# Kernel tuning notes

Measured on AMD Instinct MI355X. Metric: run time of the kernel, lower is better.

The kernel has to match this reference:

```python
import jax, jax.numpy as jnp
import numpy as np

DIM = 512
TEMB_DIM = 512
NUM_HEADS = 16
WS = 16  # window_size
N = WS * WS
B = 256


def _relative_position_index(ws: int) -> np.ndarray:
    """Swin-style relative position index, shape [ws*ws, ws*ws], values in [0, (2ws-1)^2)."""
    coords = np.stack(np.meshgrid(np.arange(ws), np.arange(ws), indexing='ij'))  # [2, ws, ws]
    flat = coords.reshape(2, -1)                                                  # [2, N]
    rel = flat[:, :, None] - flat[:, None, :]                                     # [2, N, N]
    rel = rel.transpose(1, 2, 0).copy()                                           # [N, N, 2]
    rel[:, :, 0] += ws - 1
    rel[:, :, 1] += ws - 1
    rel[:, :, 0] *= 2 * ws - 1
    return rel.sum(-1).astype(np.int32)


def setup_inputs() -> dict:
    key = jax.random.key(0)
    ks = jax.random.split(key, 8)
    lin = lambda k, fan_in, shape: jax.random.normal(k, shape, jnp.float32) * (1.0 / np.sqrt(fan_in))
    return {
        'x': jax.random.normal(ks[0], (B, N, DIM), jnp.float32),
        'temb': jax.random.normal(ks[1], (B, TEMB_DIM), jnp.float32),
        'qkv_w': lin(ks[2], DIM, (DIM, 3 * DIM)),
        'qkv_b': jnp.zeros((3 * DIM,), jnp.float32),
        'temb_w': lin(ks[3], TEMB_DIM, (TEMB_DIM, 3 * DIM)),
        'temb_b': jnp.zeros((3 * DIM,), jnp.float32),
        'rpb_table': jax.random.normal(ks[4], ((2 * WS - 1) ** 2, NUM_HEADS), jnp.float32) * 0.02,
        'proj_w': lin(ks[5], DIM, (DIM, DIM)),
        'proj_b': jnp.zeros((DIM,), jnp.float32),
        'rp_index': jnp.asarray(_relative_position_index(WS)),
    }


def reference(x, temb, qkv_w, qkv_b, temb_w, temb_b, rpb_table, proj_w, proj_b, rp_index):
    Bq, Nq, C = x.shape
    H = NUM_HEADS
    hd = C // H
    # qkv with time-embedding modulation: [B, N, 3C]
    qkv = x @ qkv_w + qkv_b + (temb @ temb_w + temb_b)[:, None, :]
    qkv = qkv.reshape(Bq, Nq, 3, H, hd).transpose(2, 0, 3, 1, 4)  # [3, B, H, N, hd]
    q, k, v = qkv[0], qkv[1], qkv[2]
    # relative position bias: [H, N, N]
    bias = rpb_table[rp_index.reshape(-1)].reshape(Nq, Nq, H).transpose(2, 0, 1)
    scale = 1.0 / jnp.sqrt(jnp.asarray(hd, x.dtype))  # SDPA default scale
    scores = jnp.einsum('bhqd,bhkd->bhqk', q, k) * scale + bias[None]
    attn = jax.nn.softmax(scores, axis=-1)
    out = jnp.einsum('bhqk,bhkd->bhqd', attn, v)       # [B, H, N, hd]
    out = out.transpose(0, 2, 1, 3).reshape(Bq, Nq, C)
    return out @ proj_w + proj_b
```

## Files before the change

kernel.cpp:

```cpp
#include <hip/hip_runtime.h>
#include <hip/hip_bf16.h>

#define B_ 256
#define N_ 256
#define H_ 16
#define SCALE2_ 0.25504526484f
#define LOG2E_ 1.4426950408889634f

typedef __attribute__((ext_vector_type(8))) short short8;
typedef __attribute__((ext_vector_type(4))) float f32x4v;
typedef unsigned int u32;

#define GLOAD16(gptr, lptr)                                                        \
  __builtin_amdgcn_global_load_lds((const __attribute__((address_space(1))) u32*)(gptr), \
                                   (__attribute__((address_space(3))) u32*)(lptr), 16, 0, 0)

static __device__ __forceinline__ unsigned cvt_pk_bf16(float lo, float hi) {
  unsigned r;
  asm("v_cvt_pk_bf16_f32 %0, %1, %2" : "=v"(r) : "v"(lo), "v"(hi));
  return r;
}

__global__ void cvt_x_kernel(const float* __restrict__ in, unsigned* __restrict__ out, int n8) {
  int i = blockIdx.x * 256 + threadIdx.x;
  int stride = gridDim.x * 256;
  for (; i < n8; i += stride) {
    const float4* p = reinterpret_cast<const float4*>(in + (size_t)i * 8);
    float4 a = p[0], b = p[1];
    uint4 vv = make_uint4(cvt_pk_bf16(a.x, a.y), cvt_pk_bf16(a.z, a.w),
                          cvt_pk_bf16(b.x, b.y), cvt_pk_bf16(b.z, b.w));
    *reinterpret_cast<uint4*>(out + (size_t)i * 4) = vv;
  }
}

__global__ void cvt_wT_kernel(const float* __restrict__ in, unsigned short* __restrict__ out, int ncols) {
  __shared__ float tile[32][65];
  const int nb = ncols >> 6;
  const int k0 = (blockIdx.x / nb) << 5;
  const int n0 = (blockIdx.x % nb) << 6;
  const int t = threadIdx.x;
  {
    int kk = t >> 3, c0 = (t & 7) << 3;
    const float* src = in + (size_t)(k0 + kk) * ncols + n0 + c0;
    float4 v0 = *reinterpret_cast<const float4*>(src);
    float4 v1 = *reinterpret_cast<const float4*>(src + 4);
    tile[kk][c0 + 0] = v0.x; tile[kk][c0 + 1] = v0.y; tile[kk][c0 + 2] = v0.z; tile[kk][c0 + 3] = v0.w;
    tile[kk][c0 + 4] = v1.x; tile[kk][c0 + 5] = v1.y; tile[kk][c0 + 6] = v1.z; tile[kk][c0 + 7] = v1.w;
  }
  __syncthreads();
  {
    int nn = t >> 2, c0 = (t & 3) << 3;
    uint4 vv = make_uint4(cvt_pk_bf16(tile[c0 + 0][nn], tile[c0 + 1][nn]),
                          cvt_pk_bf16(tile[c0 + 2][nn], tile[c0 + 3][nn]),
                          cvt_pk_bf16(tile[c0 + 4][nn], tile[c0 + 5][nn]),
                          cvt_pk_bf16(tile[c0 + 6][nn], tile[c0 + 7][nn]));
    *reinterpret_cast<uint4*>(out + (size_t)(n0 + nn) * 512 + k0 + c0) = vv;
  }
}

__global__ __launch_bounds__(512)
void temb_mod_kernel(const float* __restrict__ temb,
                     const float* __restrict__ temb_w,
                     const float* __restrict__ temb_b,
                     const float* __restrict__ qkv_b,
                     float* __restrict__ tm) {
  __shared__ float ts[512];
  const int b = blockIdx.x, t = threadIdx.x;
  ts[t] = temb[(size_t)b * 512 + t];
  __syncthreads();
  float a0 = temb_b[t] + qkv_b[t];
  float a1 = temb_b[t + 512] + qkv_b[t + 512];
  float a2 = temb_b[t + 1024] + qkv_b[t + 1024];
#pragma unroll 4
  for (int k = 0; k < 512; ++k) {
    const float tv = ts[k];
    const float* wr = temb_w + (size_t)k * 1536 + t;
    a0 += tv * wr[0];
    a1 += tv * wr[512];
    a2 += tv * wr[1024];
  }
  float* o = tm + (size_t)b * 1536 + t;
  o[0] = a0; o[512] = a1; o[1024] = a2;
}

__global__ __launch_bounds__(512, 4)
void fused_attn_kernel(const unsigned short* __restrict__ xb16,
                       const unsigned short* __restrict__ wT,
                       const float* __restrict__ rpb,
                       const float* __restrict__ tm,
                       unsigned short* __restrict__ attn_out) {
  __shared__ __align__(16) char smem[53008];
  short* xs  = (short*)smem;
  short* ksp = (short*)(smem + 16384);
  short* vTs = (short*)(smem + 32768);
  float* biasT = (float*)(smem + 49152);

  const int u = blockIdx.x;
  const int bh = ((u & 7) << 9) | (u >> 3);
  const int b = bh >> 4, h = bh & 15;
  const int tid = threadIdx.x;
  const int w = tid >> 6, l = tid & 63;
  const int l16 = l & 15, g = l >> 4;
  const int gsw8 = (g ^ ((l16 >> 1) & 3)) << 3;
  const int lrow = l >> 2;
  const int lcol = (((l & 3) ^ ((l >> 3) & 3)) << 3);

  const unsigned short* xsrc0 = xb16 + (size_t)(b * 256 + w * 16 + lrow) * 512 + lcol;
  const unsigned short* xsrc1 = xsrc0 + (size_t)128 * 512;
  const int row96 = w * 16 + lrow;
  const unsigned short* wsrc = wT + (size_t)((row96 >> 5) * 512 + h * 32 + (row96 & 31)) * 512 + lcol;

  f32x4v acc[2][6];
#pragma unroll
  for (int mt = 0; mt < 2; ++mt)
#pragma unroll
    for (int nt = 0; nt < 6; ++nt) acc[mt][nt] = (f32x4v)(0.0f);

  auto stage = [&](int t, int bufi) {
    const int k0 = t << 5;
    GLOAD16(xsrc0 + k0, xs + bufi * 8192 + w * 512);
    GLOAD16(xsrc1 + k0, xs + bufi * 8192 + (8 + w) * 512);
    if (w < 6) GLOAD16(wsrc + k0, xs + 16384 + bufi * 3072 + w * 512);
  };
  stage(0, 0);
  __syncthreads();
#pragma unroll
  for (int t = 0; t < 16; ++t) {
    const int cur = t & 1;
    if (t < 15) stage(t + 1, cur ^ 1);
    short* xb = xs + cur * 8192;
    short* wb = xs + 16384 + cur * 3072;
    short8 af[2], bfr[6];
#pragma unroll
    for (int mt = 0; mt < 2; ++mt)
      af[mt] = *reinterpret_cast<short8*>(&xb[(w * 32 + mt * 16 + l16) * 32 + gsw8]);
#pragma unroll
    for (int nt = 0; nt < 6; ++nt)
      bfr[nt] = *reinterpret_cast<short8*>(&wb[(nt * 16 + l16) * 32 + gsw8]);
#pragma unroll
    for (int mt = 0; mt < 2; ++mt)
#pragma unroll
      for (int nt = 0; nt < 6; ++nt)
        acc[mt][nt] = __builtin_amdgcn_mfma_f32_16x16x32_bf16(af[mt], bfr[nt], acc[mt][nt], 0, 0, 0);
    __syncthreads();
  }

  const float* tmb = tm + (size_t)b * 1536 + h * 32;
#pragma unroll
  for (int nt = 0; nt < 6; ++nt) {
    const int prt = nt >> 1;
    const int d = ((nt & 1) << 4) + l16;
    const float tmv = tmb[(prt << 9) + d];
#pragma unroll
    for (int mt = 0; mt < 2; ++mt) {
      const int r0 = w * 32 + mt * 16 + g * 4;
      float v0 = acc[mt][nt][0] + tmv, v1 = acc[mt][nt][1] + tmv;
      float v2 = acc[mt][nt][2] + tmv, v3 = acc[mt][nt][3] + tmv;
      if (prt == 0) { v0 *= SCALE2_; v1 *= SCALE2_; v2 *= SCALE2_; v3 *= SCALE2_; }
      const u32 p01 = cvt_pk_bf16(v0, v1);
      const u32 p23 = cvt_pk_bf16(v2, v3);
      if (prt != 2) {
        short* dst = (prt == 0) ? xs : ksp;
        const int unit01 = ((d >> 3) ^ ((r0 >> 1) & 3)) << 3;
        const int base = r0 * 32 + unit01 + (d & 7);
        dst[base]            = (short)p01;
        dst[base + 32]       = (short)(p01 >> 16);
        dst[(base + 64) ^ 8] = (short)p23;
        dst[(base + 96) ^ 8] = (short)(p23 >> 16);
      } else {
#pragma unroll
        for (int j = 0; j < 4; ++j) {
          const int key = r0 + j;
          const int vcol = ((key >> 5) << 5) | (((key & 15) << 1) | ((key >> 4) & 1));
          const int unit = ((vcol >> 3) ^ (d & 7));
          const u32 pk = (j < 2) ? p01 : p23;
          vTs[d * 256 + (unit << 3) + (vcol & 7)] = (short)(pk >> ((j & 1) << 4));
        }
      }
    }
  }
  for (int e = tid; e < 961; e += 512) biasT[e] = rpb[e * 16 + h] * LOG2E_;
  __syncthreads();

  short8 bq[2];
#pragma unroll
  for (int mt = 0; mt < 2; ++mt)
    bq[mt] = *reinterpret_cast<short8*>(&xs[(w * 32 + mt * 16 + l16) * 32 + gsw8]);

  const int bcol = l16 - (g << 2) + 15;
  const int brow0 = w * 2 + 15;

  f32x4v bp_prev;
#pragma unroll
  for (int j = 0; j < 4; ++j) bp_prev[j] = biasT[(brow0 + 1) * 31 + bcol - j];

  short8 ones8;
#pragma unroll
  for (int j = 0; j < 8; ++j) ones8[j] = (short)0x3F80;

  f32x4v oacc[2][2];
  f32x4v oaccL[2];
#pragma unroll
  for (int mt = 0; mt < 2; ++mt) {
    oacc[mt][0] = (f32x4v)(0.0f);
    oacc[mt][1] = (f32x4v)(0.0f);
    oaccL[mt] = (f32x4v)(0.0f);
  }

#pragma unroll
  for (int kc = 0; kc < 8; ++kc) {
    const int kt0 = kc * 2, kt1 = kc * 2 + 1;
    short8 kf0 = *reinterpret_cast<short8*>(&ksp[(kt0 * 16 + l16) * 32 + gsw8]);
    short8 kf1 = *reinterpret_cast<short8*>(&ksp[(kt1 * 16 + l16) * 32 + gsw8]);
    f32x4v cA, cB;
    const float* brA = biasT + (brow0 - kt0) * 31 + bcol;
    const float* brB = biasT + (brow0 - kt1) * 31 + bcol;
#pragma unroll
    for (int j = 0; j < 4; ++j) { cA[j] = brA[-j]; cB[j] = brB[-j]; }
    f32x4v s00, s01, s10, s11;
    __builtin_amdgcn_s_setprio(1);
    s00 = __builtin_amdgcn_mfma_f32_16x16x32_bf16(kf0, bq[0], cA, 0, 0, 0);
    s01 = __builtin_amdgcn_mfma_f32_16x16x32_bf16(kf0, bq[1], bp_prev, 0, 0, 0);
    s10 = __builtin_amdgcn_mfma_f32_16x16x32_bf16(kf1, bq[0], cB, 0, 0, 0);
    s11 = __builtin_amdgcn_mfma_f32_16x16x32_bf16(kf1, bq[1], cA, 0, 0, 0);
    __builtin_amdgcn_s_setprio(0);
    bp_prev = cB;

    short8 pa0, pa1;
    {
      union { u32 u[4]; short8 s8; } pk0, pk1;
#pragma unroll
      for (int j = 0; j < 4; ++j) {
        pk0.u[j] = cvt_pk_bf16(exp2f(s00[j]), exp2f(s10[j]));
        pk1.u[j] = cvt_pk_bf16(exp2f(s01[j]), exp2f(s11[j]));
      }
      pa0 = pk0.s8; pa1 = pk1.s8;
    }
    short8 bv0 = *reinterpret_cast<short8*>(
        &vTs[(l16) * 256 + ((((kc * 4 + g) ^ (l16 & 7)) << 3))]);
    short8 bv1 = *reinterpret_cast<short8*>(
        &vTs[(16 + l16) * 256 + ((((kc * 4 + g) ^ (l16 & 7)) << 3))]);
    __builtin_amdgcn_s_setprio(1);
    oacc[0][0] = __builtin_amdgcn_mfma_f32_16x16x32_bf16(pa0, bv0, oacc[0][0], 0, 0, 0);
    oacc[0][1] = __builtin_amdgcn_mfma_f32_16x16x32_bf16(pa0, bv1, oacc[0][1], 0, 0, 0);
    oacc[1][0] = __builtin_amdgcn_mfma_f32_16x16x32_bf16(pa1, bv0, oacc[1][0], 0, 0, 0);
    oacc[1][1] = __builtin_amdgcn_mfma_f32_16x16x32_bf16(pa1, bv1, oacc[1][1], 0, 0, 0);
    oaccL[0]   = __builtin_amdgcn_mfma_f32_16x16x32_bf16(pa0, ones8, oaccL[0], 0, 0, 0);
    oaccL[1]   = __builtin_amdgcn_mfma_f32_16x16x32_bf16(pa1, ones8, oaccL[1], 0, 0, 0);
    __builtin_amdgcn_s_setprio(0);
  }

  float i0[4], i1[4];
#pragma unroll
  for (int j = 0; j < 4; ++j) {
    i0[j] = __builtin_amdgcn_rcpf(oaccL[0][j]);
    i1[j] = __builtin_amdgcn_rcpf(oaccL[1][j]);
  }
  short* ob = xs + w * 1024;
  const int u0 = (((l16 >> 3) ^ g) << 3) + (l16 & 7);
  const int u1 = ((((l16 >> 3) | 2) ^ g) << 3) + (l16 & 7);
  {
    const u32 a01 = cvt_pk_bf16(oacc[0][0][0] * i0[0], oacc[0][0][1] * i0[1]);
    const u32 a23 = cvt_pk_bf16(oacc[0][0][2] * i0[2], oacc[0][0][3] * i0[3]);
    const u32 b01 = cvt_pk_bf16(oacc[0][1][0] * i0[0], oacc[0][1][1] * i0[1]);
    const u32 b23 = cvt_pk_bf16(oacc[0][1][2] * i0[2], oacc[0][1][3] * i0[3]);
    const u32 c01 = cvt_pk_bf16(oacc[1][0][0] * i1[0], oacc[1][0][1] * i1[1]);
    const u32 c23 = cvt_pk_bf16(oacc[1][0][2] * i1[2], oacc[1][0][3] * i1[3]);
    const u32 d01 = cvt_pk_bf16(oacc[1][1][0] * i1[0], oacc[1][1][1] * i1[1]);
    const u32 d23 = cvt_pk_bf16(oacc[1][1][2] * i1[2], oacc[1][1][3] * i1[3]);
    const int r0 = (g << 2) * 32;
    ob[r0 + u0]       = (short)a01;  ob[r0 + 32 + u0]  = (short)(a01 >> 16);
    ob[r0 + 64 + u0]  = (short)a23;  ob[r0 + 96 + u0]  = (short)(a23 >> 16);
    ob[r0 + u1]       = (short)b01;  ob[r0 + 32 + u1]  = (short)(b01 >> 16);
    ob[r0 + 64 + u1]  = (short)b23;  ob[r0 + 96 + u1]  = (short)(b23 >> 16);
    const int r1 = r0 + 512;
    ob[r1 + u0]       = (short)c01;  ob[r1 + 32 + u0]  = (short)(c01 >> 16);
    ob[r1 + 64 + u0]  = (short)c23;  ob[r1 + 96 + u0]  = (short)(c23 >> 16);
    ob[r1 + u1]       = (short)d01;  ob[r1 + 32 + u1]  = (short)(d01 >> 16);
    ob[r1 + 64 + u1]  = (short)d23;  ob[r1 + 96 + u1]  = (short)(d23 >> 16);
  }
  unsigned short* aw = attn_out + (size_t)(b * 256 + w * 32) * 512 + h * 32;
#pragma unroll
  for (int i = 0; i < 2; ++i) {
    const int r = i * 16 + (l >> 2);
    const int cu = l & 3;
    const int su = cu ^ ((r >> 2) & 3);
    short8 vv = *reinterpret_cast<short8*>(&ob[r * 32 + (su << 3)]);
    *reinterpret_cast<short8*>(aw + (size_t)r * 512 + (cu << 3)) = vv;
  }
}

__global__ __launch_bounds__(256)
void proj_kernel(const unsigned short* __restrict__ A,
                 const unsigned short* __restrict__ BT,
                 const float* __restrict__ proj_b,
                 float* __restrict__ out) {
  __shared__ short As[2][4096];
  __shared__ short Bs[2][4096];
  const int bid = blockIdx.x;
  const int m0 = (bid & 511) << 7, n0 = (bid >> 9) << 7;
  const int tid = threadIdx.x;
  const int w = tid >> 6, l = tid & 63, l16 = l & 15, g = l >> 4;
  const int wr = w >> 1, wc = w & 1;
  const int gsw8 = (g ^ ((l16 >> 1) & 3)) << 3;
  const int lrow = l >> 2;
  const int lcol = (((l & 3) ^ ((l >> 3) & 3)) << 3);

  const unsigned short* asrc0 = A + (size_t)(m0 + w * 16 + lrow) * 512 + lcol;
  const unsigned short* asrc1 = asrc0 + (size_t)64 * 512;
  const unsigned short* bsrc0 = BT + (size_t)(n0 + w * 16 + lrow) * 512 + lcol;
  const unsigned short* bsrc1 = bsrc0 + (size_t)64 * 512;

  f32x4v acc[4][4];
#pragma unroll
  for (int mt = 0; mt < 4; ++mt)
#pragma unroll
    for (int nt = 0; nt < 4; ++nt) acc[mt][nt] = (f32x4v)(0.0f);

  auto stage = [&](int t, int bufi) {
    const int k0 = t << 5;
    GLOAD16(asrc0 + k0, As[bufi] + w * 512);
    GLOAD16(asrc1 + k0, As[bufi] + (4 + w) * 512);
    GLOAD16(bsrc0 + k0, Bs[bufi] + w * 512);
    GLOAD16(bsrc1 + k0, Bs[bufi] + (4 + w) * 512);
  };
  stage(0, 0);
  __syncthreads();
#pragma unroll
  for (int t = 0; t < 16; ++t) {
    const int cur = t & 1;
    if (t < 15) stage(t + 1, cur ^ 1);
    short8 af[4], bfr[4];
#pragma unroll
    for (int mt = 0; mt < 4; ++mt)
      af[mt] = *reinterpret_cast<short8*>(&As[cur][(wr * 64 + mt * 16 + l16) * 32 + gsw8]);
#pragma unroll
    for (int nt = 0; nt < 4; ++nt)
      bfr[nt] = *reinterpret_cast<short8*>(&Bs[cur][(wc * 64 + nt * 16 + l16) * 32 + gsw8]);
#pragma unroll
    for (int mt = 0; mt < 4; ++mt)
#pragma unroll
      for (int nt = 0; nt < 4; ++nt)
        acc[mt][nt] = __builtin_amdgcn_mfma_f32_16x16x32_bf16(af[mt], bfr[nt], acc[mt][nt], 0, 0, 0);
    __syncthreads();
  }
#pragma unroll
  for (int nt = 0; nt < 4; ++nt) {
    const int col = n0 + wc * 64 + nt * 16 + l16;
    const float pb = proj_b[col];
#pragma unroll
    for (int mt = 0; mt < 4; ++mt)
#pragma unroll
      for (int j = 0; j < 4; ++j)
        out[(size_t)(m0 + wr * 64 + mt * 16 + g * 4 + j) * 512 + col] = acc[mt][nt][j] + pb;
  }
}

extern "C" void kernel_launch(void* const* d_in, const int* in_sizes, int n_in,
                              void* d_out, int out_size, void* d_ws, size_t ws_size,
                              hipStream_t stream) {
  const float* x      = (const float*)d_in[0];
  const float* temb   = (const float*)d_in[1];
  const float* qkv_w  = (const float*)d_in[2];
  const float* qkv_b  = (const float*)d_in[3];
  const float* temb_w = (const float*)d_in[4];
  const float* temb_b = (const float*)d_in[5];
  const float* rpb    = (const float*)d_in[6];
  const float* proj_w = (const float*)d_in[7];
  const float* proj_b = (const float*)d_in[8];
  float* out = (float*)d_out;

  char* ws = (char*)d_ws;
  float* tm               = (float*)ws;
  unsigned short* xb16    = (unsigned short*)(ws + 1572864);
  unsigned short* qkv_wT  = (unsigned short*)(ws + 1572864 + 67108864);
  unsigned short* proj_wT = (unsigned short*)(ws + 1572864 + 67108864 + 1572864);
  unsigned short* attn_ws = (unsigned short*)(ws + 1572864 + 67108864 + 1572864 + 524288);

  temb_mod_kernel<<<256, 512, 0, stream>>>(temb, temb_w, temb_b, qkv_b, tm);
  cvt_x_kernel<<<2048, 256, 0, stream>>>(x, (unsigned*)xb16, (256 * 256 * 512) / 8);
  cvt_wT_kernel<<<16 * 24, 256, 0, stream>>>(qkv_w, qkv_wT, 1536);
  cvt_wT_kernel<<<16 * 8, 256, 0, stream>>>(proj_w, proj_wT, 512);
  fused_attn_kernel<<<B_ * H_, 512, 0, stream>>>(xb16, qkv_wT, rpb, tm, attn_ws);
  proj_kernel<<<512 * 4, 256, 0, stream>>>(attn_ws, proj_wT, proj_b, out);
}
```

Baseline: 363.3 us.

## Merge prep kernels, triple-buffer QKV GEMM loads, swizzle proj block order

Replaces four preprocessing launches (temb modulation, x conversion, two weight transposes) with one prep kernel dispatched by block index, removing launch gaps. The fused attention kernel's QKV GEMM moves from double to triple buffering with explicit vmcnt waits and one barrier per step, so loads run further ahead of the MFMAs. The shared-memory footprint grows to about 66KB, which may reduce occupancy. The projection GEMM remaps block IDs so blocks that run together share A rows for better L2 reuse.

```diff
diff --git a/kernel.cpp b/kernel.cpp
--- a/kernel.cpp
+++ b/kernel.cpp
@@ -21,66 +21,75 @@
   return r;
 }
 
-__global__ void cvt_x_kernel(const float* __restrict__ in, unsigned* __restrict__ out, int n8) {
-  int i = blockIdx.x * 256 + threadIdx.x;
-  int stride = gridDim.x * 256;
-  for (; i < n8; i += stride) {
-    const float4* p = reinterpret_cast<const float4*>(in + (size_t)i * 8);
-    float4 a = p[0], b = p[1];
-    uint4 vv = make_uint4(cvt_pk_bf16(a.x, a.y), cvt_pk_bf16(a.z, a.w),
-                          cvt_pk_bf16(b.x, b.y), cvt_pk_bf16(b.z, b.w));
-    *reinterpret_cast<uint4*>(out + (size_t)i * 4) = vv;
-  }
-}
-
-__global__ void cvt_wT_kernel(const float* __restrict__ in, unsigned short* __restrict__ out, int ncols) {
-  __shared__ float tile[32][65];
-  const int nb = ncols >> 6;
-  const int k0 = (blockIdx.x / nb) << 5;
-  const int n0 = (blockIdx.x % nb) << 6;
+__global__ __launch_bounds__(512)
+void prep_kernel(const float* __restrict__ temb, const float* __restrict__ temb_w,
+                 const float* __restrict__ temb_b, const float* __restrict__ qkv_b,
+                 float* __restrict__ tm,
+                 const float* __restrict__ x, unsigned* __restrict__ xb16,
+                 const float* __restrict__ qkv_w, unsigned short* __restrict__ qkv_wT,
+                 const float* __restrict__ proj_w, unsigned short* __restrict__ proj_wT) {
+  __shared__ __align__(16) char lbuf[17024];
+  const int blk = blockIdx.x;
   const int t = threadIdx.x;
-  {
-    int kk = t >> 3, c0 = (t & 7) << 3;
-    const float* src = in + (size_t)(k0 + kk) * ncols + n0 + c0;
-    float4 v0 = *reinterpret_cast<const float4*>(src);
-    float4 v1 = *reinterpret_cast<const float4*>(src + 4);
-    tile[kk][c0 + 0] = v0.x; tile[kk][c0 + 1] = v0.y; tile[kk][c0 + 2] = v0.z; tile[kk][c0 + 3] = v0.w;
-    tile[kk][c0 + 4] = v1.x; tile[kk][c0 + 5] = v1.y; tile[kk][c0 + 6] = v1.z; tile[kk][c0 + 7] = v1.w;
-  }
-  __syncthreads();
-  {
-    int nn = t >> 2, c0 = (t & 3) << 3;
-    uint4 vv = make_uint4(cvt_pk_bf16(tile[c0 + 0][nn], tile[c0 + 1][nn]),
-                          cvt_pk_bf16(tile[c0 + 2][nn], tile[c0 + 3][nn]),
-                          cvt_pk_bf16(tile[c0 + 4][nn], tile[c0 + 5][nn]),
-                          cvt_pk_bf16(tile[c0 + 6][nn], tile[c0 + 7][nn]));
-    *reinterpret_cast<uint4*>(out + (size_t)(n0 + nn) * 512 + k0 + c0) = vv;
-  }
-}
-
-__global__ __launch_bounds__(512)
-void temb_mod_kernel(const float* __restrict__ temb,
-                     const float* __restrict__ temb_w,
-                     const float* __restrict__ temb_b,
-                     const float* __restrict__ qkv_b,
-                     float* __restrict__ tm) {
-  __shared__ float ts[512];
-  const int b = blockIdx.x, t = threadIdx.x;
-  ts[t] = temb[(size_t)b * 512 + t];
-  __syncthreads();
-  float a0 = temb_b[t] + qkv_b[t];
-  float a1 = temb_b[t + 512] + qkv_b[t + 512];
-  float a2 = temb_b[t + 1024] + qkv_b[t + 1024];
+
+  if (blk < 256) {
+    float* ts = (float*)lbuf;
+    const int b = blk;
+    ts[t] = temb[(size_t)b * 512 + t];
+    __syncthreads();
+    float a0 = temb_b[t] + qkv_b[t];
+    float a1 = temb_b[t + 512] + qkv_b[t + 512];
+    float a2 = temb_b[t + 1024] + qkv_b[t + 1024];
 #pragma unroll 4
-  for (int k = 0; k < 512; ++k) {
-    const float tv = ts[k];
-    const float* wr = temb_w + (size_t)k * 1536 + t;
-    a0 += tv * wr[0];
-    a1 += tv * wr[512];
-    a2 += tv * wr[1024];
-  }
-  float* o = tm + (size_t)b * 1536 + t;
-  o[0] = a0; o[512] = a1; o[1024] = a2;
+    for (int k = 0; k < 512; ++k) {
+      const float tv = ts[k];
+      const float* wr = temb_w + (size_t)k * 1536 + t;
+      a0 += tv * wr[0];
+      a1 += tv * wr[512];
+      a2 += tv * wr[1024];
+    }
+    float* o = tm + (size_t)b * 1536 + t;
+    o[0] = a0; o[512] = a1; o[1024] = a2;
+  } else if (blk < 1280) {
+    const int n8 = (B_ * N_ * 512) / 8;
+    int i = (blk - 256) * 512 + t;
+    for (; i < n8; i += 1024 * 512) {
+      const float4* p = reinterpret_cast<const float4*>(x + (size_t)i * 8);
+      float4 a = p[0], b4 = p[1];
+      uint4 vv = make_uint4(cvt_pk_bf16(a.x, a.y), cvt_pk_bf16(a.z, a.w),
+                            cvt_pk_bf16(b4.x, b4.y), cvt_pk_bf16(b4.z, b4.w));
+      *reinterpret_cast<uint4*>(xb16 + (size_t)i * 4) = vv;
+    }
+  } else {
+    const float* src; unsigned short* dst; int ncols, k0, n0;
+    if (blk < 1472) {
+      const int idx = blk - 1280;
+      src = qkv_w; dst = qkv_wT; ncols = 1536;
+      k0 = (idx / 12) << 5; n0 = (idx % 12) << 7;
+    } else {
+      const int idx = blk - 1472;
+      src = proj_w; dst = proj_wT; ncols = 512;
+      k0 = (idx >> 2) << 5; n0 = (idx & 3) << 7;
+    }
+    float (*tile)[133] = (float (*)[133])lbuf;
+    {
+      const int kk = t >> 4, c0 = (t & 15) << 3;
+      const float* s = src + (size_t)(k0 + kk) * ncols + n0 + c0;
+      float4 v0 = *reinterpret_cast<const float4*>(s);
+      float4 v1 = *reinterpret_cast<const float4*>(s + 4);
+      tile[kk][c0 + 0] = v0.x; tile[kk][c0 + 1] = v0.y; tile[kk][c0 + 2] = v0.z; tile[kk][c0 + 3] = v0.w;
+      tile[kk][c0 + 4] = v1.x; tile[kk][c0 + 5] = v1.y; tile[kk][c0 + 6] = v1.z; tile[kk][c0 + 7] = v1.w;
+    }
+    __syncthreads();
+    {
+      const int nn = t >> 2, ck = (t & 3) << 3;
+      uint4 vv = make_uint4(cvt_pk_bf16(tile[ck + 0][nn], tile[ck + 1][nn]),
+                            cvt_pk_bf16(tile[ck + 2][nn], tile[ck + 3][nn]),
+                            cvt_pk_bf16(tile[ck + 4][nn], tile[ck + 5][nn]),
+                            cvt_pk_bf16(tile[ck + 6][nn], tile[ck + 7][nn]));
+      *reinterpret_cast<uint4*>(dst + (size_t)(n0 + nn) * 512 + k0 + ck) = vv;
+    }
+  }
 }
 
 __global__ __launch_bounds__(512, 4)
@@ -89,11 +98,12 @@
                        const float* __restrict__ rpb,
                        const float* __restrict__ tm,
                        unsigned short* __restrict__ attn_out) {
-  __shared__ __align__(16) char smem[53008];
-  short* xs  = (short*)smem;
-  short* ksp = (short*)(smem + 16384);
-  short* vTs = (short*)(smem + 32768);
-  float* biasT = (float*)(smem + 49152);
+  __shared__ __align__(16) char smem[67584];
+  short* xs     = (short*)smem;
+  short* ksp    = (short*)(smem + 16384);
+  short* vTs    = (short*)(smem + 32768);
+  short* wstage = (short*)(smem + 49152);
+  float* biasT  = (float*)(smem + 49152);
 
   const int u = blockIdx.x;
   const int bh = ((u & 7) << 9) | (u >> 3);
@@ -120,16 +130,24 @@
     const int k0 = t << 5;
     GLOAD16(xsrc0 + k0, xs + bufi * 8192 + w * 512);
     GLOAD16(xsrc1 + k0, xs + bufi * 8192 + (8 + w) * 512);
-    if (w < 6) GLOAD16(wsrc + k0, xs + 16384 + bufi * 3072 + w * 512);
+    if (w < 6) GLOAD16(wsrc + k0, wstage + bufi * 3072 + w * 512);
   };
   stage(0, 0);
-  __syncthreads();
 #pragma unroll
   for (int t = 0; t < 16; ++t) {
-    const int cur = t & 1;
-    if (t < 15) stage(t + 1, cur ^ 1);
-    short* xb = xs + cur * 8192;
-    short* wb = xs + 16384 + cur * 3072;
+    const int buf = t % 3;
+    if (t < 15) {
+      stage(t + 1, (t + 1) % 3);
+      if (w < 6) asm volatile("s_waitcnt vmcnt(3)" ::: "memory");
+      else       asm volatile("s_waitcnt vmcnt(2)" ::: "memory");
+    } else {
+      asm volatile("s_waitcnt vmcnt(0)" ::: "memory");
+    }
+    __builtin_amdgcn_sched_barrier(0);
+    __builtin_amdgcn_s_barrier();
+    __builtin_amdgcn_sched_barrier(0);
+    short* xb = xs + buf * 8192;
+    short* wb = wstage + buf * 3072;
     short8 af[2], bfr[6];
 #pragma unroll
     for (int mt = 0; mt < 2; ++mt)
@@ -142,8 +160,8 @@
 #pragma unroll
       for (int nt = 0; nt < 6; ++nt)
         acc[mt][nt] = __builtin_amdgcn_mfma_f32_16x16x32_bf16(af[mt], bfr[nt], acc[mt][nt], 0, 0, 0);
-    __syncthreads();
-  }
+  }
+  __syncthreads();
 
   const float* tmb = tm + (size_t)b * 1536 + h * 32;
 #pragma unroll
@@ -297,8 +315,10 @@
                  float* __restrict__ out) {
   __shared__ short As[2][4096];
   __shared__ short Bs[2][4096];
-  const int bid = blockIdx.x;
-  const int m0 = (bid & 511) << 7, n0 = (bid >> 9) << 7;
+  const int bid0 = blockIdx.x;
+  const int swz = ((bid0 & 7) << 8) | (bid0 >> 3);
+  const int m0 = (swz >> 2) << 7;
+  const int n0 = (swz & 3) << 7;
   const int tid = threadIdx.x;
   const int w = tid >> 6, l = tid & 63, l16 = l & 15, g = l >> 4;
   const int wr = w >> 1, wc = w & 1;
@@ -377,10 +397,9 @@
   unsigned short* proj_wT = (unsigned short*)(ws + 1572864 + 67108864 + 1572864);
   unsigned short* attn_ws = (unsigned short*)(ws + 1572864 + 67108864 + 1572864 + 524288);
 
-  temb_mod_kernel<<<256, 512, 0, stream>>>(temb, temb_w, temb_b, qkv_b, tm);
-  cvt_x_kernel<<<2048, 256, 0, stream>>>(x, (unsigned*)xb16, (256 * 256 * 512) / 8);
-  cvt_wT_kernel<<<16 * 24, 256, 0, stream>>>(qkv_w, qkv_wT, 1536);
-  cvt_wT_kernel<<<16 * 8, 256, 0, stream>>>(proj_w, proj_wT, 512);
+  prep_kernel<<<1536, 512, 0, stream>>>(temb, temb_w, temb_b, qkv_b, tm,
+                                        x, (unsigned*)xb16,
+                                        qkv_w, qkv_wT, proj_w, proj_wT);
   fused_attn_kernel<<<B_ * H_, 512, 0, stream>>>(xb16, qkv_wT, rpb, tm, attn_ws);
-  proj_kernel<<<512 * 4, 256, 0, stream>>>(attn_ws, proj_wT, proj_b, out);
+  proj_kernel<<<2048, 256, 0, stream>>>(attn_ws, proj_wT, proj_b, out);
 }
```

Measured after the change: 334.0 us. 1.09x faster.
